# Performance work log

Measured on AMD Instinct MI355X. Metric: run time of the kernel, lower is better.

## Reference

```python
import jax, jax.numpy as jnp
import numpy as np

RADIUS = 5
KS = 2 * RADIUS - 1          # kernel_size = 9
PAD = KS // 2                # 4
CENTER = RADIUS - 1          # 4 (== PAD)
EPS = 1e-10


def _offsets_and_kernel():
    # Distance kernel exactly as torch.meshgrid(indexing='ij') in the module;
    # the center entry is skipped in the loop, so drop it here.
    yy, xx = np.meshgrid(np.arange(KS), np.arange(KS), indexing='ij')
    dist = np.sqrt((xx - CENTER) ** 2 + (yy - CENTER) ** 2).astype(np.float32)
    keep = ~((yy == CENTER) & (xx == CENTER))
    return (yy[keep].astype(np.int32), xx[keep].astype(np.int32), dist[keep])


def setup_inputs() -> dict:
    key = jax.random.key(0)
    target = (jax.random.uniform(key, (5, 2048, 2048)) < 0.15).astype(jnp.float32)
    return {"target": target}


def reference(target):
    # target: [5, H, W] binary float masks
    H, W = target.shape[1], target.shape[2]
    feature_weight = jnp.sum(target, axis=0)                      # [H, W]
    combined = (feature_weight > 0).astype(jnp.float32)           # [H, W]

    padded = jnp.pad(combined, PAD, mode='edge')                  # replicate pad
    oi, oj, kv = _offsets_and_kernel()
    offs = (jnp.asarray(oi), jnp.asarray(oj), jnp.asarray(kv))

    def body(min_d, off):
        i, j, k = off
        shifted = jax.lax.dynamic_slice(padded, (i, j), (H, W))
        diff = (shifted != combined).astype(jnp.float32)
        d = jnp.where(diff > 0, k / (diff + EPS), jnp.inf)
        return jnp.minimum(min_d, d), None

    min_d, _ = jax.lax.scan(body, jnp.full((H, W), jnp.inf, jnp.float32), offs)

    contour = jnp.where(jnp.isfinite(min_d), 1.0 / (min_d + EPS), 0.0)
    w = (feature_weight + contour) ** 2
    w = (w - w.min()) / (w.max() - w.min() + EPS)
    return w * combined
```

## Files before the change

kernel.cpp:

```cpp
#include <hip/hip_runtime.h>
#include <math.h>
#include <utility>

static constexpr int HH = 2048;
static constexpr int WW = 2048;
static constexpr int NPIX = HH * WW;
static constexpr int WPR32 = WW / 32;
static constexpr int NWAVE_DIST = 2048;

template <typename F, int... Is>
__device__ __forceinline__ void sf_impl(F&& f, std::integer_sequence<int, Is...>) {
    (f(std::integral_constant<int, Is>{}), ...);
}
template <int N, typename F>
__device__ __forceinline__ void static_for(F&& f) {
    sf_impl(f, std::make_integer_sequence<int, N>{});
}

__host__ __device__ constexpr int rank_of(int d2) {
    switch (d2) {
        case 1:  return 1;  case 2:  return 2;  case 4:  return 3;
        case 5:  return 4;  case 8:  return 5;  case 9:  return 6;
        case 10: return 7;  case 13: return 8;  case 16: return 9;
        case 17: return 10; case 18: return 11; case 20: return 12;
        case 25: return 13; case 32: return 14;
    }
    return 0;
}

__device__ const int D2S[16] = {0, 1, 2, 4, 5, 8, 9, 10, 13, 16, 17, 18, 20, 25, 32, 0};

__device__ __forceinline__ unsigned long long spread8(unsigned int b) {
    unsigned long long t = (unsigned long long)b * 0x0101010101010101ull;
    t &= 0x8040201008040201ull;
    return ((t + 0x7f7f7f7f7f7f7f7full) >> 7) & 0x0101010101010101ull;
}

__global__ __launch_bounds__(256) void k_pack(const float* __restrict__ t,
                                              unsigned char* __restrict__ fw,
                                              unsigned char* __restrict__ pk) {
    const int tid = blockIdx.x * 256 + threadIdx.x;
    const int base = tid * 8;
    unsigned long long fwq = 0;
    unsigned int bits = 0;
#pragma unroll
    for (int h = 0; h < 2; ++h) {
        const int o = base + 4 * h;
        float4 a = *(const float4*)(t + 0 * NPIX + o);
        float4 b = *(const float4*)(t + 1 * NPIX + o);
        float4 c = *(const float4*)(t + 2 * NPIX + o);
        float4 d = *(const float4*)(t + 3 * NPIX + o);
        float4 e = *(const float4*)(t + 4 * NPIX + o);
        const float s0 = a.x + b.x + c.x + d.x + e.x;
        const float s1 = a.y + b.y + c.y + d.y + e.y;
        const float s2 = a.z + b.z + c.z + d.z + e.z;
        const float s3 = a.w + b.w + c.w + d.w + e.w;
        const int j = 4 * h;
        fwq |= ((unsigned long long)(int)s0) << (8 * j);
        fwq |= ((unsigned long long)(int)s1) << (8 * (j + 1));
        fwq |= ((unsigned long long)(int)s2) << (8 * (j + 2));
        fwq |= ((unsigned long long)(int)s3) << (8 * (j + 3));
        bits |= (s0 > 0.f ? 1u : 0u) << j;
        bits |= (s1 > 0.f ? 1u : 0u) << (j + 1);
        bits |= (s2 > 0.f ? 1u : 0u) << (j + 2);
        bits |= (s3 > 0.f ? 1u : 0u) << (j + 3);
    }
    *(unsigned long long*)(fw + base) = fwq;
    pk[tid] = (unsigned char)bits;
}

__global__ __launch_bounds__(512) void k_dist(const unsigned* __restrict__ pk32,
                                              const unsigned long long* __restrict__ fw8,
                                              unsigned long long* __restrict__ code8,
                                              unsigned long long* __restrict__ obs_slots) {
    __shared__ unsigned tile[16][WPR32];

    const int y0 = blockIdx.x * 8;
#pragma unroll
    for (int k = 0; k < 2; ++k) {
        const int idx = threadIdx.x + k * 512;
        const int r = idx >> 6;
        const int wx = idx & 63;
        const int gy = min(max(y0 - 4 + r, 0), HH - 1);
        tile[r][wx] = pk32[gy * WPR32 + wx];
    }
    __syncthreads();

    const int ty = threadIdx.x >> 6;
    const int wx = threadIdx.x & 63;
    const int t = (y0 + ty) * WPR32 + wx;

    unsigned acc[15];
    static_for<15>([&](auto I) { acc[I.value] = 0u; });

    const unsigned C = tile[ty + 4][wx];

    static_for<9>([&](auto DY) {
        constexpr int dy = DY.value - 4;
        const int r = ty + dy + 4;
        const unsigned M = tile[r][wx];
        const unsigned L = (wx > 0) ? tile[r][wx - 1] : ((M & 1u) ? ~0u : 0u);
        const unsigned R = (wx < WPR32 - 1) ? tile[r][wx + 1]
                                            : ((M >> 31) ? ~0u : 0u);
        static_for<9>([&](auto DX) {
            constexpr int dx = DX.value - 4;
            if constexpr (!(dx == 0 && dy == 0)) {
                constexpr int rk = rank_of(dy * dy + dx * dx);
                unsigned S;
                if constexpr (dx > 0)      S = (M >> dx) | (R << (32 - dx));
                else if constexpr (dx < 0) S = (M << (-dx)) | (L >> (32 + dx));
                else                       S = M;
                acc[rk] |= S ^ C;
            }
        });
    });

    unsigned found = 0, p0 = 0, p1 = 0, p2 = 0, p3 = 0;
    static_for<14>([&](auto RI) {
        constexpr int r = RI.value + 1;
        const unsigned nw = acc[r] & ~found;
        found |= acc[r];
        if constexpr (r & 1) p0 |= nw;
        if constexpr (r & 2) p1 |= nw;
        if constexpr (r & 4) p2 |= nw;
        if constexpr (r & 8) p3 |= nw;
    });

    unsigned long long lo = 0, hi = 0;
    static_for<4>([&](auto J) {
        constexpr int j = J.value;
        const unsigned long long f = fw8[t * 4 + j];
        const unsigned int c0 = (p0 >> (8 * j)) & 0xff;
        const unsigned int c1 = (p1 >> (8 * j)) & 0xff;
        const unsigned int c2 = (p2 >> (8 * j)) & 0xff;
        const unsigned int c3 = (p3 >> (8 * j)) & 0xff;
        const unsigned long long cls = spread8(c0) | (spread8(c1) << 1)
                                     | (spread8(c2) << 2) | (spread8(c3) << 3);
        const unsigned long long cq = (f << 4) | cls;
        code8[t * 4 + j] = cq;
        static_for<8>([&](auto B) {
            constexpr int b = B.value;
            const unsigned int code = (unsigned int)((cq >> (8 * b)) & 0xff);
            const unsigned long long bit = 1ull << (code & 63);
            const bool ishi = (code & 64) != 0;
            lo |= ishi ? 0ull : bit;
            hi |= ishi ? bit : 0ull;
        });
    });

#pragma unroll
    for (int s = 32; s > 0; s >>= 1) {
        lo |= __shfl_xor(lo, s);
        hi |= __shfl_xor(hi, s);
    }
    if ((threadIdx.x & 63) == 0) {
        const int wave = blockIdx.x * 8 + (threadIdx.x >> 6);
        obs_slots[wave * 2]     = lo;
        obs_slots[wave * 2 + 1] = hi;
    }
}

__global__ __launch_bounds__(256) void k_out(const unsigned long long* __restrict__ code8,
                                             const unsigned long long* __restrict__ obs_slots,
                                             float* __restrict__ out) {
    __shared__ float tab[96];
    __shared__ float smn[4], smx[4];
    __shared__ unsigned long long slo[4], shi[4];

    const int tid = threadIdx.x;

    unsigned long long lo = 0, hi = 0;
    {
        const ulonglong2* sl2 = (const ulonglong2*)obs_slots;
#pragma unroll
        for (int i = 0; i < 8; ++i) {
            const ulonglong2 s = sl2[tid * 8 + i];
            lo |= s.x;
            hi |= s.y;
        }
#pragma unroll
        for (int s = 32; s > 0; s >>= 1) {
            lo |= __shfl_xor(lo, s);
            hi |= __shfl_xor(hi, s);
        }
        if ((tid & 63) == 0) { slo[tid >> 6] = lo; shi[tid >> 6] = hi; }
        __syncthreads();
        lo = slo[0] | slo[1] | slo[2] | slo[3];
        hi = shi[0] | shi[1] | shi[2] | shi[3];
    }

    float v = 0.f;
    bool present = false;
    if (tid < 96) {
        const int r = tid & 15;
        const float contour = (r >= 1 && r <= 14) ? 1.f / sqrtf((float)D2S[r]) : 0.f;
        const float t0 = (float)(tid >> 4) + contour;
        v = t0 * t0;
        present = (tid < 64) ? ((lo >> tid) & 1) : ((hi >> (tid - 64)) & 1);
    }
    float mnv = present ? v : INFINITY;
    float mxv = present ? v : -INFINITY;
#pragma unroll
    for (int s = 32; s > 0; s >>= 1) {
        mnv = fminf(mnv, __shfl_xor(mnv, s));
        mxv = fmaxf(mxv, __shfl_xor(mxv, s));
    }
    if ((tid & 63) == 0) { smn[tid >> 6] = mnv; smx[tid >> 6] = mxv; }
    __syncthreads();
    const float mn = fminf(fminf(smn[0], smn[1]), fminf(smn[2], smn[3]));
    const float mx = fmaxf(fmaxf(smx[0], smx[1]), fmaxf(smx[2], smx[3]));
    const float inv = 1.f / (mx - mn + 1e-10f);
    if (tid < 96) tab[tid] = (tid >= 16) ? (v - mn) * inv : 0.f;
    __syncthreads();

    const int t = blockIdx.x * 256 + tid;
    const unsigned long long cq = code8[t];
    float4 v0, v1;
    v0.x = tab[(cq >> 0) & 0xff];
    v0.y = tab[(cq >> 8) & 0xff];
    v0.z = tab[(cq >> 16) & 0xff];
    v0.w = tab[(cq >> 24) & 0xff];
    v1.x = tab[(cq >> 32) & 0xff];
    v1.y = tab[(cq >> 40) & 0xff];
    v1.z = tab[(cq >> 48) & 0xff];
    v1.w = tab[(cq >> 56) & 0xff];
    *(float4*)(out + t * 8) = v0;
    *(float4*)(out + t * 8 + 4) = v1;
}

extern "C" void kernel_launch(void* const* d_in, const int* in_sizes, int n_in,
                              void* d_out, int out_size, void* d_ws, size_t ws_size,
                              hipStream_t stream) {
    const float* target = (const float*)d_in[0];
    float* out = (float*)d_out;

    unsigned char* fw = (unsigned char*)d_ws;
    unsigned char* pk = fw + NPIX;
    unsigned char* code = pk + NPIX / 8;
    unsigned long long* obs_slots = (unsigned long long*)(code + NPIX);

    k_pack<<<NPIX / 8 / 256, 256, 0, stream>>>(target, fw, pk);

    k_dist<<<HH / 8, 512, 0, stream>>>(
        (const unsigned*)pk, (const unsigned long long*)fw,
        (unsigned long long*)code, obs_slots);

    k_out<<<NPIX / 8 / 256, 256, 0, stream>>>(
        (const unsigned long long*)code, obs_slots, out);
}
```

Measured before the change: 38.08 us.

## Split distance work into 16-bit halves per thread and pre-reduce observed codes per block

k_dist now uses 1024 threads per block, and each thread handles 16 pixels instead of 32. It builds a 64-bit window so every shift becomes a single 64-bit shift, and it issues its feature-weight load before the barrier. The observed-code bitmask is reduced across the whole block before being written, so k_out reads one slot per block instead of summing per-wave slots. k_out also handles 16 pixels per thread with wider loads and stores, in half as many blocks. The aim is more parallelism and less reduction traffic, at the cost of larger blocks and redundant mask work for the upper 16 bits of each word.

Result: faster. 36.81 us (-3.3%).

```diff
diff --git a/kernel.cpp b/kernel.cpp
--- a/kernel.cpp
+++ b/kernel.cpp
@@ -6,7 +6,7 @@
 static constexpr int WW = 2048;
 static constexpr int NPIX = HH * WW;
 static constexpr int WPR32 = WW / 32;
-static constexpr int NWAVE_DIST = 2048;
+static constexpr int HPR = WW / 16;
 
 template <typename F, int... Is>
 __device__ __forceinline__ void sf_impl(F&& f, std::integer_sequence<int, Is...>) {
@@ -69,47 +69,55 @@
     pk[tid] = (unsigned char)bits;
 }
 
-__global__ __launch_bounds__(512) void k_dist(const unsigned* __restrict__ pk32,
-                                              const unsigned long long* __restrict__ fw8,
-                                              unsigned long long* __restrict__ code8,
-                                              unsigned long long* __restrict__ obs_slots) {
+__global__ __launch_bounds__(1024) void k_dist(const unsigned* __restrict__ pk32,
+                                               const ulonglong2* __restrict__ fw16,
+                                               ulonglong2* __restrict__ code16,
+                                               unsigned long long* __restrict__ obs_blk) {
     __shared__ unsigned tile[16][WPR32];
+    __shared__ unsigned long long swl[16], swh[16];
 
     const int y0 = blockIdx.x * 8;
-#pragma unroll
-    for (int k = 0; k < 2; ++k) {
-        const int idx = threadIdx.x + k * 512;
-        const int r = idx >> 6;
-        const int wx = idx & 63;
+    {
+        const int r = threadIdx.x >> 6;
+        const int c = threadIdx.x & 63;
         const int gy = min(max(y0 - 4 + r, 0), HH - 1);
-        tile[r][wx] = pk32[gy * WPR32 + wx];
-    }
-    __syncthreads();
-
-    const int ty = threadIdx.x >> 6;
-    const int wx = threadIdx.x & 63;
-    const int t = (y0 + ty) * WPR32 + wx;
+        tile[r][c] = pk32[gy * WPR32 + c];
+    }
+
+    const int ty = threadIdx.x >> 7;
+    const int hx = threadIdx.x & 127;
+    const int wx = hx >> 1;
+    const int h = hx & 1;
+    const int chunk = (y0 + ty) * HPR + hx;
+
+    const ulonglong2 fv2 = fw16[chunk];
+
+    __syncthreads();
 
     unsigned acc[15];
     static_for<15>([&](auto I) { acc[I.value] = 0u; });
 
-    const unsigned C = tile[ty + 4][wx];
+    const unsigned Cw = tile[ty + 4][wx];
+    const unsigned C = h ? (Cw >> 16) : (Cw & 0xffffu);
 
     static_for<9>([&](auto DY) {
         constexpr int dy = DY.value - 4;
         const int r = ty + dy + 4;
         const unsigned M = tile[r][wx];
-        const unsigned L = (wx > 0) ? tile[r][wx - 1] : ((M & 1u) ? ~0u : 0u);
-        const unsigned R = (wx < WPR32 - 1) ? tile[r][wx + 1]
-                                            : ((M >> 31) ? ~0u : 0u);
+        unsigned long long W;
+        if (h == 0) {
+            const unsigned P = (wx > 0) ? tile[r][wx - 1] : ((M & 1u) ? ~0u : 0u);
+            W = ((unsigned long long)M << 4) | (P >> 28);
+        } else {
+            const unsigned N = (wx < WPR32 - 1) ? tile[r][wx + 1]
+                                                : ((M >> 31) ? ~0u : 0u);
+            W = ((unsigned long long)N << 20) | (M >> 12);
+        }
         static_for<9>([&](auto DX) {
             constexpr int dx = DX.value - 4;
             if constexpr (!(dx == 0 && dy == 0)) {
                 constexpr int rk = rank_of(dy * dy + dx * dx);
-                unsigned S;
-                if constexpr (dx > 0)      S = (M >> dx) | (R << (32 - dx));
-                else if constexpr (dx < 0) S = (M << (-dx)) | (L >> (32 + dx));
-                else                       S = M;
+                const unsigned S = (unsigned)(W >> (4 + dx));
                 acc[rk] |= S ^ C;
             }
         });
@@ -126,42 +134,55 @@
         if constexpr (r & 8) p3 |= nw;
     });
 
+    unsigned long long cq0 = 0, cq1 = 0;
     unsigned long long lo = 0, hi = 0;
-    static_for<4>([&](auto J) {
+    static_for<2>([&](auto J) {
         constexpr int j = J.value;
-        const unsigned long long f = fw8[t * 4 + j];
-        const unsigned int c0 = (p0 >> (8 * j)) & 0xff;
-        const unsigned int c1 = (p1 >> (8 * j)) & 0xff;
-        const unsigned int c2 = (p2 >> (8 * j)) & 0xff;
-        const unsigned int c3 = (p3 >> (8 * j)) & 0xff;
+        const unsigned long long f = j ? fv2.y : fv2.x;
+        const unsigned c0 = (p0 >> (8 * j)) & 0xff;
+        const unsigned c1 = (p1 >> (8 * j)) & 0xff;
+        const unsigned c2 = (p2 >> (8 * j)) & 0xff;
+        const unsigned c3 = (p3 >> (8 * j)) & 0xff;
         const unsigned long long cls = spread8(c0) | (spread8(c1) << 1)
                                      | (spread8(c2) << 2) | (spread8(c3) << 3);
         const unsigned long long cq = (f << 4) | cls;
-        code8[t * 4 + j] = cq;
+        if constexpr (j == 0) cq0 = cq; else cq1 = cq;
         static_for<8>([&](auto B) {
             constexpr int b = B.value;
-            const unsigned int code = (unsigned int)((cq >> (8 * b)) & 0xff);
+            const unsigned code = (unsigned)((cq >> (8 * b)) & 0xff);
             const unsigned long long bit = 1ull << (code & 63);
             const bool ishi = (code & 64) != 0;
             lo |= ishi ? 0ull : bit;
             hi |= ishi ? bit : 0ull;
         });
     });
+    code16[chunk] = make_ulonglong2(cq0, cq1);
 
 #pragma unroll
     for (int s = 32; s > 0; s >>= 1) {
         lo |= __shfl_xor(lo, s);
         hi |= __shfl_xor(hi, s);
     }
-    if ((threadIdx.x & 63) == 0) {
-        const int wave = blockIdx.x * 8 + (threadIdx.x >> 6);
-        obs_slots[wave * 2]     = lo;
-        obs_slots[wave * 2 + 1] = hi;
-    }
-}
-
-__global__ __launch_bounds__(256) void k_out(const unsigned long long* __restrict__ code8,
-                                             const unsigned long long* __restrict__ obs_slots,
+    const int wid = threadIdx.x >> 6;
+    if ((threadIdx.x & 63) == 0) { swl[wid] = lo; swh[wid] = hi; }
+    __syncthreads();
+    if (threadIdx.x < 64) {
+        unsigned long long l2 = (threadIdx.x < 16) ? swl[threadIdx.x] : 0ull;
+        unsigned long long h2 = (threadIdx.x < 16) ? swh[threadIdx.x] : 0ull;
+#pragma unroll
+        for (int s = 8; s > 0; s >>= 1) {
+            l2 |= __shfl_xor(l2, s);
+            h2 |= __shfl_xor(h2, s);
+        }
+        if (threadIdx.x == 0) {
+            obs_blk[blockIdx.x * 2] = l2;
+            obs_blk[blockIdx.x * 2 + 1] = h2;
+        }
+    }
+}
+
+__global__ __launch_bounds__(256) void k_out(const ulonglong2* __restrict__ code16,
+                                             const unsigned long long* __restrict__ obs_blk,
                                              float* __restrict__ out) {
     __shared__ float tab[96];
     __shared__ float smn[4], smx[4];
@@ -169,19 +190,15 @@
 
     const int tid = threadIdx.x;
 
-    unsigned long long lo = 0, hi = 0;
+    unsigned long long lo, hi;
     {
-        const ulonglong2* sl2 = (const ulonglong2*)obs_slots;
-#pragma unroll
-        for (int i = 0; i < 8; ++i) {
-            const ulonglong2 s = sl2[tid * 8 + i];
-            lo |= s.x;
-            hi |= s.y;
-        }
-#pragma unroll
-        for (int s = 32; s > 0; s >>= 1) {
-            lo |= __shfl_xor(lo, s);
-            hi |= __shfl_xor(hi, s);
+        const ulonglong2 s = ((const ulonglong2*)obs_blk)[tid];
+        lo = s.x;
+        hi = s.y;
+#pragma unroll
+        for (int s2 = 32; s2 > 0; s2 >>= 1) {
+            lo |= __shfl_xor(lo, s2);
+            hi |= __shfl_xor(hi, s2);
         }
         if ((tid & 63) == 0) { slo[tid >> 6] = lo; shi[tid >> 6] = hi; }
         __syncthreads();
@@ -214,18 +231,21 @@
     __syncthreads();
 
     const int t = blockIdx.x * 256 + tid;
-    const unsigned long long cq = code8[t];
-    float4 v0, v1;
-    v0.x = tab[(cq >> 0) & 0xff];
-    v0.y = tab[(cq >> 8) & 0xff];
-    v0.z = tab[(cq >> 16) & 0xff];
-    v0.w = tab[(cq >> 24) & 0xff];
-    v1.x = tab[(cq >> 32) & 0xff];
-    v1.y = tab[(cq >> 40) & 0xff];
-    v1.z = tab[(cq >> 48) & 0xff];
-    v1.w = tab[(cq >> 56) & 0xff];
-    *(float4*)(out + t * 8) = v0;
-    *(float4*)(out + t * 8 + 4) = v1;
+    const ulonglong2 cq = code16[t];
+    float4 v0, v1, v2, v3;
+    v0.x = tab[(cq.x >> 0) & 0xff];  v0.y = tab[(cq.x >> 8) & 0xff];
+    v0.z = tab[(cq.x >> 16) & 0xff]; v0.w = tab[(cq.x >> 24) & 0xff];
+    v1.x = tab[(cq.x >> 32) & 0xff]; v1.y = tab[(cq.x >> 40) & 0xff];
+    v1.z = tab[(cq.x >> 48) & 0xff]; v1.w = tab[(cq.x >> 56) & 0xff];
+    v2.x = tab[(cq.y >> 0) & 0xff];  v2.y = tab[(cq.y >> 8) & 0xff];
+    v2.z = tab[(cq.y >> 16) & 0xff]; v2.w = tab[(cq.y >> 24) & 0xff];
+    v3.x = tab[(cq.y >> 32) & 0xff]; v3.y = tab[(cq.y >> 40) & 0xff];
+    v3.z = tab[(cq.y >> 48) & 0xff]; v3.w = tab[(cq.y >> 56) & 0xff];
+    const int ob = t * 16;
+    *(float4*)(out + ob + 0)  = v0;
+    *(float4*)(out + ob + 4)  = v1;
+    *(float4*)(out + ob + 8)  = v2;
+    *(float4*)(out + ob + 12) = v3;
 }
 
 extern "C" void kernel_launch(void* const* d_in, const int* in_sizes, int n_in,
@@ -237,14 +257,14 @@
     unsigned char* fw = (unsigned char*)d_ws;
     unsigned char* pk = fw + NPIX;
     unsigned char* code = pk + NPIX / 8;
-    unsigned long long* obs_slots = (unsigned long long*)(code + NPIX);
+    unsigned long long* obs_blk = (unsigned long long*)(code + NPIX);
 
     k_pack<<<NPIX / 8 / 256, 256, 0, stream>>>(target, fw, pk);
 
-    k_dist<<<HH / 8, 512, 0, stream>>>(
-        (const unsigned*)pk, (const unsigned long long*)fw,
-        (unsigned long long*)code, obs_slots);
-
-    k_out<<<NPIX / 8 / 256, 256, 0, stream>>>(
-        (const unsigned long long*)code, obs_slots, out);
-}
+    k_dist<<<HH / 8, 1024, 0, stream>>>(
+        (const unsigned*)pk, (const ulonglong2*)fw,
+        (ulonglong2*)code, obs_blk);
+
+    k_out<<<NPIX / 16 / 256, 256, 0, stream>>>(
+        (const ulonglong2*)code, obs_blk, out);
+}
```
